# Kernel optimization log

Measured on AMD Instinct MI355X. Metric: run time of the kernel, lower is better.

Reference implementation:

```python
import jax, jax.numpy as jnp
import numpy as np

B, H, S, D = 4, 16, 2048, 64

def setup_inputs() -> dict:
    key = jax.random.key(0)
    kq, kk, kv = jax.random.split(key, 3)
    Q = jax.random.normal(kq, (B, H, S, D), dtype=jnp.float32)
    K = jax.random.normal(kk, (B, H, S, D), dtype=jnp.float32)
    V = jax.random.normal(kv, (B, H, S, D), dtype=jnp.float32)
    return {"Q": Q, "K": K, "V": V}

def reference(Q, K, V):
    d = Q.shape[-1]
    scale = jnp.sqrt(jnp.asarray(d, dtype=Q.dtype))
    # scores: [B, H, S, S]
    scores = jnp.einsum('bhqd,bhkd->bhqk', Q, K) / scale
    attn = jax.nn.softmax(scores, axis=-1)
    out = jnp.einsum('bhqk,bhkd->bhqd', attn, V)  # [B,H,S,D]
    # permute to [B,S,H,D] then merge heads -> [B,S,H*D]
    b, h, s, dd = out.shape
    return out.transpose(0, 2, 1, 3).reshape(b, s, h * dd)
```

## Files before the change

kernel.cpp:

```cpp
#include <hip/hip_runtime.h>
#include <hip/hip_bf16.h>


#define B_ 4
#define H_ 16
#define S_ 2048
#define D_ 64
#define BH 64
#define NKT 32
#define TILE_USH 4096
#define ARR_USH ((size_t)BH * NKT * TILE_USH)
#define WS_NEED (2 * ARR_USH * 2)
#define QSCALE 0.18033688011112042f

typedef float  f4 __attribute__((ext_vector_type(4)));
typedef short  s4 __attribute__((ext_vector_type(4)));
typedef short  s8 __attribute__((ext_vector_type(8)));
typedef unsigned short ushort_t;

__device__ __forceinline__ unsigned short f2bf(float x) {
  unsigned int u = __float_as_uint(x);
  u += 0x7fffu + ((u >> 16) & 1u);
  return (unsigned short)(u >> 16);
}
__device__ __forceinline__ unsigned int pk_bf16(float a, float b) {
  __hip_bfloat162 h = __float22bfloat162_rn(make_float2(a, b));
  union { __hip_bfloat162 h2; unsigned int u; } cv; cv.h2 = h; return cv.u;
}
__device__ __forceinline__ void splitbf_rne(float x, unsigned short& hi, unsigned short& lo) {
  hi = f2bf(x);
  float hf = __uint_as_float((unsigned int)hi << 16);
  lo = f2bf(x - hf);
}
__device__ __forceinline__ void splitbf(float x, unsigned short& hi, unsigned short& lo) {
  unsigned int u = __float_as_uint(x);
  hi = (unsigned short)(u >> 16);
  float hf = __uint_as_float(u & 0xffff0000u);
  lo = (unsigned short)(__float_as_uint(x - hf) >> 16);
}

typedef __attribute__((address_space(1))) const unsigned int* gas_t;
typedef __attribute__((address_space(3))) unsigned int* las_t;
__device__ __forceinline__ void gl_lds16(const void* g, void* l) {
  __builtin_amdgcn_global_load_lds((gas_t)g, (las_t)l, 16, 0, 0);
}

__global__ __launch_bounds__(256)
void prep(const float* __restrict__ K, const float* __restrict__ V,
          ushort_t* __restrict__ KH, ushort_t* __restrict__ VT) {
  __shared__ float Vf[64][68];
  const int tile = blockIdx.x;
  const int t = threadIdx.x;

  const float* vsrc = V + (size_t)tile * 4096;
  float4 vv[4];
  int srow[4], dcol[4];
  #pragma unroll
  for (int r = 0; r < 4; ++r) {
    int f = r * 256 + t; srow[r] = f >> 4; dcol[r] = (f & 15) << 2;
    vv[r] = *(const float4*)(vsrc + srow[r] * 64 + dcol[r]);
  }
  {
    const float* src0 = K + (size_t)tile * 4096;
    #pragma unroll
    for (int u = 0; u < 2; ++u) {
      unsigned int i = u * 256 + t;
      unsigned int row = i >> 3, c = (i & 7) ^ (row & 7);
      const float* src = src0 + row * 64 + c * 8;
      float4 a = *(const float4*)src;
      float4 b = *(const float4*)(src + 4);
      unsigned int d0 = pk_bf16(a.x, a.y), d1 = pk_bf16(a.z, a.w);
      unsigned int d2 = pk_bf16(b.x, b.y), d3 = pk_bf16(b.z, b.w);
      uint4 out = make_uint4(d0, d1, d2, d3);
      *(uint4*)(KH + (size_t)tile * TILE_USH + i * 8) = out;
    }
  }
  #pragma unroll
  for (int r = 0; r < 4; ++r) {
    int pcol = dcol[r] ^ (((srow[r] >> 3) & 3) << 2);
    *(float4*)&Vf[srow[r]][pcol] = vv[r];
  }
  __syncthreads();
  #pragma unroll
  for (int u = 0; u < 2; ++u) {
    unsigned int i = u * 256 + t;
    unsigned int drow = i >> 3, c = (i & 7) ^ (drow & 7);
    const unsigned int ka   = ((c >> 2) << 5) + ((c & 3) << 2);
    const unsigned int colA = drow ^ ((c & 2) << 1);
    const unsigned int colB = colA ^ 8;
    unsigned int d0 = pk_bf16(Vf[ka +  0][colA], Vf[ka +  1][colA]);
    unsigned int d1 = pk_bf16(Vf[ka +  2][colA], Vf[ka +  3][colA]);
    unsigned int d2 = pk_bf16(Vf[ka + 16][colB], Vf[ka + 17][colB]);
    unsigned int d3 = pk_bf16(Vf[ka + 18][colB], Vf[ka + 19][colB]);
    uint4 out = make_uint4(d0, d1, d2, d3);
    *(uint4*)(VT + (size_t)tile * TILE_USH + i * 8) = out;
  }
}

__global__ __launch_bounds__(256, 4)
void attn10(const float* __restrict__ Q, const ushort_t* __restrict__ KH,
            const ushort_t* __restrict__ VT, float* __restrict__ O) {
  __shared__ ushort_t KhS[2][TILE_USH];
  __shared__ ushort_t VtS[2][TILE_USH];

  const int t    = threadIdx.x;
  const int w    = t >> 6;
  const int lane = t & 63;
  const int g    = lane >> 4;
  const int ln   = lane & 15;

  const unsigned int n = blockIdx.x;
  const int bh = (int)((n >> 7) * 8 + (n & 7));
  const int q0 = (int)(((n >> 3) & 15) * 128);

  const size_t tb = (size_t)bh * NKT * TILE_USH;
  const unsigned int cb = w * 128;

  #pragma unroll
  for (int j = 0; j < 2; ++j) {
    const unsigned int ch = cb + 64u * j;
    const size_t go = tb + (size_t)(ch + lane) * 8;
    gl_lds16(KH + go, &KhS[0][ch * 8]);
    gl_lds16(VT + go, &VtS[0][ch * 8]);
  }

  s8 qfh[2][2], qfl[2][2];
  #pragma unroll
  for (int sub = 0; sub < 2; ++sub) {
    const int q = q0 + 32 * w + 16 * sub + ln;
    #pragma unroll
    for (int ks = 0; ks < 2; ++ks) {
      const float* qp = Q + ((size_t)bh * S_ + q) * 64 + 32 * ks + 8 * g;
      float4 a = *(const float4*)qp;
      float4 b = *(const float4*)(qp + 4);
      float xs[8] = {a.x, a.y, a.z, a.w, b.x, b.y, b.z, b.w};
      s8 hv, lv;
      #pragma unroll
      for (int j = 0; j < 8; ++j) {
        unsigned short h, lo; splitbf_rne(xs[j] * QSCALE, h, lo);
        hv[j] = (short)h; lv[j] = (short)lo;
      }
      qfh[sub][ks] = hv; qfl[sub][ks] = lv;
    }
  }

  f4 oacc[2][4];
  f4 lacc[2];
  #pragma unroll
  for (int s = 0; s < 2; ++s) {
    lacc[s] = (f4)0.0f;
    #pragma unroll
    for (int d = 0; d < 4; ++d) oacc[s][d] = (f4)0.0f;
  }

  s8 ones;
  #pragma unroll
  for (int j = 0; j < 8; ++j) ones[j] = (short)0x3F80;

  unsigned int foff[2];
  #pragma unroll
  for (int ks = 0; ks < 2; ++ks)
    foff[ks] = (unsigned)ln * 128u + (unsigned)(((4 * ks + g) ^ (ln & 7)) * 16);

  for (int kt = 0; kt < NKT; ++kt) {
    const int cur = kt & 1;
    __syncthreads();

    if (kt + 1 < NKT) {
      const size_t tbase = tb + (size_t)(kt + 1) * TILE_USH;
      const int nb = cur ^ 1;
      #pragma unroll
      for (int j = 0; j < 2; ++j) {
        const unsigned int ch = cb + 64u * j;
        const size_t go = tbase + (size_t)(ch + lane) * 8;
        gl_lds16(KH + go, &KhS[nb][ch * 8]);
        gl_lds16(VT + go, &VtS[nb][ch * 8]);
      }
    }

    const char* khb = (const char*)&KhS[cur][0];
    const char* vtb = (const char*)&VtS[cur][0];

    #pragma unroll
    for (int h = 0; h < 2; ++h) {
      s8 k00 = *(const s8*)(khb + (2 * h + 0) * 2048 + foff[0]);
      s8 k01 = *(const s8*)(khb + (2 * h + 0) * 2048 + foff[1]);
      s8 k10 = *(const s8*)(khb + (2 * h + 1) * 2048 + foff[0]);
      s8 k11 = *(const s8*)(khb + (2 * h + 1) * 2048 + foff[1]);

      s8 pa[2];
      #pragma unroll
      for (int sub = 0; sub < 2; ++sub) {
        f4 s0 = (f4)0.0f, s1 = (f4)0.0f;
        s0 = __builtin_amdgcn_mfma_f32_16x16x32_bf16(k00, qfh[sub][0], s0, 0, 0, 0);
        s0 = __builtin_amdgcn_mfma_f32_16x16x32_bf16(k00, qfl[sub][0], s0, 0, 0, 0);
        s0 = __builtin_amdgcn_mfma_f32_16x16x32_bf16(k01, qfh[sub][1], s0, 0, 0, 0);
        s0 = __builtin_amdgcn_mfma_f32_16x16x32_bf16(k01, qfl[sub][1], s0, 0, 0, 0);
        s1 = __builtin_amdgcn_mfma_f32_16x16x32_bf16(k10, qfh[sub][0], s1, 0, 0, 0);
        s1 = __builtin_amdgcn_mfma_f32_16x16x32_bf16(k10, qfl[sub][0], s1, 0, 0, 0);
        s1 = __builtin_amdgcn_mfma_f32_16x16x32_bf16(k11, qfh[sub][1], s1, 0, 0, 0);
        s1 = __builtin_amdgcn_mfma_f32_16x16x32_bf16(k11, qfl[sub][1], s1, 0, 0, 0);

        unsigned int a0 = pk_bf16(__builtin_amdgcn_exp2f(s0[0]),
                                  __builtin_amdgcn_exp2f(s0[1]));
        unsigned int a1 = pk_bf16(__builtin_amdgcn_exp2f(s0[2]),
                                  __builtin_amdgcn_exp2f(s0[3]));
        unsigned int b0 = pk_bf16(__builtin_amdgcn_exp2f(s1[0]),
                                  __builtin_amdgcn_exp2f(s1[1]));
        unsigned int b1 = pk_bf16(__builtin_amdgcn_exp2f(s1[2]),
                                  __builtin_amdgcn_exp2f(s1[3]));
        union { unsigned int u[4]; s8 v; } cvp;
        cvp.u[0] = a0; cvp.u[1] = a1; cvp.u[2] = b0; cvp.u[3] = b1;
        pa[sub] = cvp.v;
        lacc[sub] = __builtin_amdgcn_mfma_f32_16x16x32_bf16(pa[sub], ones, lacc[sub], 0, 0, 0);
      }

      #pragma unroll
      for (int dt = 0; dt < 4; ++dt) {
        s8 vb = *(const s8*)(vtb + dt * 2048 + foff[h]);
        #pragma unroll
        for (int sub = 0; sub < 2; ++sub)
          oacc[sub][dt] = __builtin_amdgcn_mfma_f32_16x16x32_bf16(pa[sub], vb, oacc[sub][dt], 0, 0, 0);
      }
    }
  }

  const int b = bh >> 4, hh = bh & 15;
  #pragma unroll
  for (int sub = 0; sub < 2; ++sub)
    #pragma unroll
    for (int r = 0; r < 4; ++r) {
      const float inv = 1.0f / lacc[sub][r];
      const int q = q0 + 32 * w + 16 * sub + 4 * g + r;
      float* dst = O + ((size_t)b * S_ + q) * (H_ * D_) + hh * 64;
      #pragma unroll
      for (int dt = 0; dt < 4; ++dt)
        dst[16 * dt + ln] = oacc[sub][dt][r] * inv;
    }
}

#define KQ_STR 72
#define VP_STR 76
__global__ __launch_bounds__(256, 2)
void attn_mfma(const float* __restrict__ Q, const float* __restrict__ K,
               const float* __restrict__ V, float* __restrict__ O) {
  __shared__ __align__(16) unsigned short Qh[64][KQ_STR];
  __shared__ __align__(16) unsigned short Ql[64][KQ_STR];
  __shared__ __align__(16) unsigned short Kh[64][KQ_STR];
  __shared__ __align__(16) unsigned short Kl[64][KQ_STR];
  __shared__ __align__(16) unsigned short Vt[64][VP_STR];
  __shared__ __align__(16) unsigned short Pb2[4][16][VP_STR];
  const int t = threadIdx.x, w = t >> 6, lane = t & 63, g = lane >> 4, ln = lane & 15;
  const int bh = blockIdx.x, q0 = blockIdx.y * 64;
  const size_t base = (size_t)bh * S_ * D_;
  {
    const float* Qg = Q + base + (size_t)q0 * D_;
    #pragma unroll
    for (int r = 0; r < 4; ++r) {
      int f = r * 256 + t, row = f >> 4, c4 = (f & 15) << 2;
      float4 v = *(const float4*)(Qg + row * 64 + c4);
      s4 hv, lv; unsigned short hb, lb;
      splitbf(v.x * 0.125f, hb, lb); hv[0] = (short)hb; lv[0] = (short)lb;
      splitbf(v.y * 0.125f, hb, lb); hv[1] = (short)hb; lv[1] = (short)lb;
      splitbf(v.z * 0.125f, hb, lb); hv[2] = (short)hb; lv[2] = (short)lb;
      splitbf(v.w * 0.125f, hb, lb); hv[3] = (short)hb; lv[3] = (short)lb;
      *(s4*)&Qh[row][c4] = hv; *(s4*)&Ql[row][c4] = lv;
    }
  }
  __syncthreads();
  s8 qfh[2], qfl[2];
  #pragma unroll
  for (int ks = 0; ks < 2; ++ks) {
    qfh[ks] = *(const s8*)&Qh[16 * w + ln][ks * 32 + 8 * g];
    qfl[ks] = *(const s8*)&Ql[16 * w + ln][ks * 32 + 8 * g];
  }
  f4 oacc[4]; float m[4], l[4];
  #pragma unroll
  for (int i = 0; i < 4; ++i) { oacc[i] = (f4)0.0f; m[i] = -1e30f; l[i] = 0.0f; }
  const float* Kg = K + base; const float* Vg = V + base;
  float4 kreg[4], vreg[4];
  #pragma unroll
  for (int r = 0; r < 4; ++r) {
    int f = r * 256 + t, row = f >> 4, c4 = (f & 15) << 2;
    kreg[r] = *(const float4*)(Kg + row * 64 + c4);
  }
  #pragma unroll
  for (int j = 0; j < 2; ++j) {
    int it = j * 256 + t, kp = it >> 4, c4 = (it & 15) << 2;
    vreg[2 * j] = *(const float4*)(Vg + (2 * kp) * 64 + c4);
    vreg[2 * j + 1] = *(const float4*)(Vg + (2 * kp + 1) * 64 + c4);
  }
  for (int kt = 0; kt < S_ / 64; ++kt) {
    __syncthreads();
    #pragma unroll
    for (int r = 0; r < 4; ++r) {
      int f = r * 256 + t, row = f >> 4, c4 = (f & 15) << 2;
      float4 v = kreg[r];
      s4 hv, lv; unsigned short hb, lb;
      splitbf(v.x, hb, lb); hv[0] = (short)hb; lv[0] = (short)lb;
      splitbf(v.y, hb, lb); hv[1] = (short)hb; lv[1] = (short)lb;
      splitbf(v.z, hb, lb); hv[2] = (short)hb; lv[2] = (short)lb;
      splitbf(v.w, hb, lb); hv[3] = (short)hb; lv[3] = (short)lb;
      *(s4*)&Kh[row][c4] = hv; *(s4*)&Kl[row][c4] = lv;
    }
    #pragma unroll
    for (int j = 0; j < 2; ++j) {
      int it = j * 256 + t, kp = it >> 4, c4 = (it & 15) << 2;
      float4 a = vreg[2 * j], b = vreg[2 * j + 1];
      float xa[4] = {a.x, a.y, a.z, a.w}, xb[4] = {b.x, b.y, b.z, b.w};
      #pragma unroll
      for (int i = 0; i < 4; ++i) {
        unsigned int pk = (unsigned int)f2bf(xa[i]) | ((unsigned int)f2bf(xb[i]) << 16);
        *(unsigned int*)&Vt[c4 + i][2 * kp] = pk;
      }
    }
    if (kt + 1 < S_ / 64) {
      const float* Kt = Kg + (size_t)(kt + 1) * 4096;
      const float* Vn = Vg + (size_t)(kt + 1) * 4096;
      #pragma unroll
      for (int r = 0; r < 4; ++r) {
        int f = r * 256 + t, row = f >> 4, c4 = (f & 15) << 2;
        kreg[r] = *(const float4*)(Kt + row * 64 + c4);
      }
      #pragma unroll
      for (int j = 0; j < 2; ++j) {
        int it = j * 256 + t, kp = it >> 4, c4 = (it & 15) << 2;
        vreg[2 * j] = *(const float4*)(Vn + (2 * kp) * 64 + c4);
        vreg[2 * j + 1] = *(const float4*)(Vn + (2 * kp + 1) * 64 + c4);
      }
    }
    __syncthreads();
    f4 sacc[4];
    #pragma unroll
    for (int nt = 0; nt < 4; ++nt) sacc[nt] = (f4)0.0f;
    #pragma unroll
    for (int nt = 0; nt < 4; ++nt)
      #pragma unroll
      for (int ks = 0; ks < 2; ++ks) {
        s8 kh = *(const s8*)&Kh[16 * nt + ln][ks * 32 + 8 * g];
        s8 kl = *(const s8*)&Kl[16 * nt + ln][ks * 32 + 8 * g];
        sacc[nt] = __builtin_amdgcn_mfma_f32_16x16x32_bf16(qfh[ks], kh, sacc[nt], 0, 0, 0);
        sacc[nt] = __builtin_amdgcn_mfma_f32_16x16x32_bf16(qfl[ks], kh, sacc[nt], 0, 0, 0);
        sacc[nt] = __builtin_amdgcn_mfma_f32_16x16x32_bf16(qfh[ks], kl, sacc[nt], 0, 0, 0);
      }
    #pragma unroll
    for (int r = 0; r < 4; ++r) {
      float rm = fmaxf(fmaxf(sacc[0][r], sacc[1][r]), fmaxf(sacc[2][r], sacc[3][r]));
      rm = fmaxf(rm, __shfl_xor(rm, 1)); rm = fmaxf(rm, __shfl_xor(rm, 2));
      rm = fmaxf(rm, __shfl_xor(rm, 4)); rm = fmaxf(rm, __shfl_xor(rm, 8));
      float mn = fmaxf(m[r], rm);
      float alpha = __expf(m[r] - mn); m[r] = mn;
      float p0 = __expf(sacc[0][r] - mn), p1 = __expf(sacc[1][r] - mn);
      float p2 = __expf(sacc[2][r] - mn), p3 = __expf(sacc[3][r] - mn);
      float rs = p0 + p1 + p2 + p3;
      rs += __shfl_xor(rs, 1); rs += __shfl_xor(rs, 2);
      rs += __shfl_xor(rs, 4); rs += __shfl_xor(rs, 8);
      l[r] = l[r] * alpha + rs;
      oacc[0][r] *= alpha; oacc[1][r] *= alpha; oacc[2][r] *= alpha; oacc[3][r] *= alpha;
      const int row = 4 * g + r;
      Pb2[w][row][ln] = f2bf(p0); Pb2[w][row][ln + 16] = f2bf(p1);
      Pb2[w][row][ln + 32] = f2bf(p2); Pb2[w][row][ln + 48] = f2bf(p3);
    }
    #pragma unroll
    for (int ks = 0; ks < 2; ++ks) {
      s4 pa0 = *(const s4*)&Pb2[w][ln][ks * 32 + 8 * g];
      s4 pa1 = *(const s4*)&Pb2[w][ln][ks * 32 + 8 * g + 4];
      s8 pa = __builtin_shufflevector(pa0, pa1, 0, 1, 2, 3, 4, 5, 6, 7);
      #pragma unroll
      for (int dt = 0; dt < 4; ++dt) {
        s4 vb0 = *(const s4*)&Vt[16 * dt + ln][ks * 32 + 8 * g];
        s4 vb1 = *(const s4*)&Vt[16 * dt + ln][ks * 32 + 8 * g + 4];
        s8 vb = __builtin_shufflevector(vb0, vb1, 0, 1, 2, 3, 4, 5, 6, 7);
        oacc[dt] = __builtin_amdgcn_mfma_f32_16x16x32_bf16(pa, vb, oacc[dt], 0, 0, 0);
      }
    }
  }
  const int b = bh >> 4, h = bh & 15;
  #pragma unroll
  for (int r = 0; r < 4; ++r) {
    const int q = q0 + 16 * w + 4 * g + r;
    const float inv = 1.0f / l[r];
    float* dst = O + ((size_t)b * S_ + q) * (H_ * D_) + h * 64;
    #pragma unroll
    for (int dt = 0; dt < 4; ++dt) dst[16 * dt + ln] = oacc[dt][r] * inv;
  }
}

extern "C" void kernel_launch(void* const* d_in, const int* in_sizes, int n_in,
                              void* d_out, int out_size, void* d_ws, size_t ws_size,
                              hipStream_t stream) {
  const float* Q = (const float*)d_in[0];
  const float* K = (const float*)d_in[1];
  const float* V = (const float*)d_in[2];
  float* Out = (float*)d_out;
  if (ws_size >= WS_NEED) {
    ushort_t* KHp = (ushort_t*)d_ws;
    ushort_t* VTp = KHp + ARR_USH;
    hipLaunchKernelGGL(prep, dim3(2048), dim3(256), 0, stream, K, V, KHp, VTp);
    hipLaunchKernelGGL(attn10, dim3(1024), dim3(256), 0, stream, Q, KHp, VTp, Out);
  } else {
    hipLaunchKernelGGL(attn_mfma, dim3(BH, S_ / 64), dim3(256), 0, stream, Q, K, V, Out);
  }
}
```

Before: 214.2 us.

## Software-pipeline QK and PV halves and raise wave priority around MFMA blocks

Restructures the per-tile inner loop so the QK^T MFMAs for the second key half are issued before the exp2/pack of the first half finishes feeding PV. This interleaves transcendental VALU work with independent MFMA chains. It also wraps each MFMA cluster in s_setprio(1)/s_setprio(0) so the arbiter favours matrix issue across co-resident waves. Holding SA and SB together raises register pressure, which could spill or lower occupancy under the 4-wave launch bound.

```diff
diff --git a/kernel.cpp b/kernel.cpp
--- a/kernel.cpp
+++ b/kernel.cpp
@@ -37,6 +37,10 @@
   hi = (unsigned short)(u >> 16);
   float hf = __uint_as_float(u & 0xffff0000u);
   lo = (unsigned short)(__float_as_uint(x - hf) >> 16);
+}
+
+__device__ __forceinline__ f4 mf(s8 a, s8 b, f4 c) {
+  return __builtin_amdgcn_mfma_f32_16x16x32_bf16(a, b, c, 0, 0, 0);
 }
 
 typedef __attribute__((address_space(1))) const unsigned int* gas_t;
@@ -98,7 +102,7 @@
 }
 
 __global__ __launch_bounds__(256, 4)
-void attn10(const float* __restrict__ Q, const ushort_t* __restrict__ KH,
+void attn11(const float* __restrict__ Q, const ushort_t* __restrict__ KH,
             const ushort_t* __restrict__ VT, float* __restrict__ O) {
   __shared__ ushort_t KhS[2][TILE_USH];
   __shared__ ushort_t VtS[2][TILE_USH];
@@ -181,47 +185,105 @@
     const char* khb = (const char*)&KhS[cur][0];
     const char* vtb = (const char*)&VtS[cur][0];
 
-    #pragma unroll
-    for (int h = 0; h < 2; ++h) {
-      s8 k00 = *(const s8*)(khb + (2 * h + 0) * 2048 + foff[0]);
-      s8 k01 = *(const s8*)(khb + (2 * h + 0) * 2048 + foff[1]);
-      s8 k10 = *(const s8*)(khb + (2 * h + 1) * 2048 + foff[0]);
-      s8 k11 = *(const s8*)(khb + (2 * h + 1) * 2048 + foff[1]);
-
-      s8 pa[2];
+    f4 SA[2][2], SB[2][2];
+    s8 paA[2], paB[2];
+
+    {
+      s8 k0 = *(const s8*)(khb + 0 * 2048 + foff[0]);
+      s8 k1 = *(const s8*)(khb + 0 * 2048 + foff[1]);
+      s8 k2 = *(const s8*)(khb + 1 * 2048 + foff[0]);
+      s8 k3 = *(const s8*)(khb + 1 * 2048 + foff[1]);
+      __builtin_amdgcn_s_setprio(1);
       #pragma unroll
       for (int sub = 0; sub < 2; ++sub) {
-        f4 s0 = (f4)0.0f, s1 = (f4)0.0f;
-        s0 = __builtin_amdgcn_mfma_f32_16x16x32_bf16(k00, qfh[sub][0], s0, 0, 0, 0);
-        s0 = __builtin_amdgcn_mfma_f32_16x16x32_bf16(k00, qfl[sub][0], s0, 0, 0, 0);
-        s0 = __builtin_amdgcn_mfma_f32_16x16x32_bf16(k01, qfh[sub][1], s0, 0, 0, 0);
-        s0 = __builtin_amdgcn_mfma_f32_16x16x32_bf16(k01, qfl[sub][1], s0, 0, 0, 0);
-        s1 = __builtin_amdgcn_mfma_f32_16x16x32_bf16(k10, qfh[sub][0], s1, 0, 0, 0);
-        s1 = __builtin_amdgcn_mfma_f32_16x16x32_bf16(k10, qfl[sub][0], s1, 0, 0, 0);
-        s1 = __builtin_amdgcn_mfma_f32_16x16x32_bf16(k11, qfh[sub][1], s1, 0, 0, 0);
-        s1 = __builtin_amdgcn_mfma_f32_16x16x32_bf16(k11, qfl[sub][1], s1, 0, 0, 0);
-
-        unsigned int a0 = pk_bf16(__builtin_amdgcn_exp2f(s0[0]),
-                                  __builtin_amdgcn_exp2f(s0[1]));
-        unsigned int a1 = pk_bf16(__builtin_amdgcn_exp2f(s0[2]),
-                                  __builtin_amdgcn_exp2f(s0[3]));
-        unsigned int b0 = pk_bf16(__builtin_amdgcn_exp2f(s1[0]),
-                                  __builtin_amdgcn_exp2f(s1[1]));
-        unsigned int b1 = pk_bf16(__builtin_amdgcn_exp2f(s1[2]),
-                                  __builtin_amdgcn_exp2f(s1[3]));
-        union { unsigned int u[4]; s8 v; } cvp;
-        cvp.u[0] = a0; cvp.u[1] = a1; cvp.u[2] = b0; cvp.u[3] = b1;
-        pa[sub] = cvp.v;
-        lacc[sub] = __builtin_amdgcn_mfma_f32_16x16x32_bf16(pa[sub], ones, lacc[sub], 0, 0, 0);
-      }
-
+        f4 x0 = (f4)0.0f, x1 = (f4)0.0f;
+        x0 = mf(k0, qfh[sub][0], x0); x0 = mf(k0, qfl[sub][0], x0);
+        x0 = mf(k1, qfh[sub][1], x0); x0 = mf(k1, qfl[sub][1], x0);
+        x1 = mf(k2, qfh[sub][0], x1); x1 = mf(k2, qfl[sub][0], x1);
+        x1 = mf(k3, qfh[sub][1], x1); x1 = mf(k3, qfl[sub][1], x1);
+        SA[sub][0] = x0; SA[sub][1] = x1;
+      }
+      __builtin_amdgcn_s_setprio(0);
+    }
+
+    #pragma unroll
+    for (int sub = 0; sub < 2; ++sub) {
+      f4 x0 = SA[sub][0], x1 = SA[sub][1];
+      unsigned int a0 = pk_bf16(__builtin_amdgcn_exp2f(x0[0]),
+                                __builtin_amdgcn_exp2f(x0[1]));
+      unsigned int a1 = pk_bf16(__builtin_amdgcn_exp2f(x0[2]),
+                                __builtin_amdgcn_exp2f(x0[3]));
+      unsigned int b0 = pk_bf16(__builtin_amdgcn_exp2f(x1[0]),
+                                __builtin_amdgcn_exp2f(x1[1]));
+      unsigned int b1 = pk_bf16(__builtin_amdgcn_exp2f(x1[2]),
+                                __builtin_amdgcn_exp2f(x1[3]));
+      union { unsigned int u[4]; s8 v; } cvp;
+      cvp.u[0] = a0; cvp.u[1] = a1; cvp.u[2] = b0; cvp.u[3] = b1;
+      paA[sub] = cvp.v;
+    }
+
+    {
+      s8 k0 = *(const s8*)(khb + 2 * 2048 + foff[0]);
+      s8 k1 = *(const s8*)(khb + 2 * 2048 + foff[1]);
+      s8 k2 = *(const s8*)(khb + 3 * 2048 + foff[0]);
+      s8 k3 = *(const s8*)(khb + 3 * 2048 + foff[1]);
+      __builtin_amdgcn_s_setprio(1);
+      #pragma unroll
+      for (int sub = 0; sub < 2; ++sub) {
+        f4 x0 = (f4)0.0f, x1 = (f4)0.0f;
+        x0 = mf(k0, qfh[sub][0], x0); x0 = mf(k0, qfl[sub][0], x0);
+        x0 = mf(k1, qfh[sub][1], x0); x0 = mf(k1, qfl[sub][1], x0);
+        x1 = mf(k2, qfh[sub][0], x1); x1 = mf(k2, qfl[sub][0], x1);
+        x1 = mf(k3, qfh[sub][1], x1); x1 = mf(k3, qfl[sub][1], x1);
+        SB[sub][0] = x0; SB[sub][1] = x1;
+      }
+      __builtin_amdgcn_s_setprio(0);
+    }
+
+    {
+      __builtin_amdgcn_s_setprio(1);
+      #pragma unroll
+      for (int sub = 0; sub < 2; ++sub)
+        lacc[sub] = mf(paA[sub], ones, lacc[sub]);
       #pragma unroll
       for (int dt = 0; dt < 4; ++dt) {
-        s8 vb = *(const s8*)(vtb + dt * 2048 + foff[h]);
+        s8 vb = *(const s8*)(vtb + dt * 2048 + foff[0]);
         #pragma unroll
         for (int sub = 0; sub < 2; ++sub)
-          oacc[sub][dt] = __builtin_amdgcn_mfma_f32_16x16x32_bf16(pa[sub], vb, oacc[sub][dt], 0, 0, 0);
-      }
+          oacc[sub][dt] = mf(paA[sub], vb, oacc[sub][dt]);
+      }
+      __builtin_amdgcn_s_setprio(0);
+    }
+
+    #pragma unroll
+    for (int sub = 0; sub < 2; ++sub) {
+      f4 x0 = SB[sub][0], x1 = SB[sub][1];
+      unsigned int a0 = pk_bf16(__builtin_amdgcn_exp2f(x0[0]),
+                                __builtin_amdgcn_exp2f(x0[1]));
+      unsigned int a1 = pk_bf16(__builtin_amdgcn_exp2f(x0[2]),
+                                __builtin_amdgcn_exp2f(x0[3]));
+      unsigned int b0 = pk_bf16(__builtin_amdgcn_exp2f(x1[0]),
+                                __builtin_amdgcn_exp2f(x1[1]));
+      unsigned int b1 = pk_bf16(__builtin_amdgcn_exp2f(x1[2]),
+                                __builtin_amdgcn_exp2f(x1[3]));
+      union { unsigned int u[4]; s8 v; } cvp;
+      cvp.u[0] = a0; cvp.u[1] = a1; cvp.u[2] = b0; cvp.u[3] = b1;
+      paB[sub] = cvp.v;
+    }
+
+    {
+      __builtin_amdgcn_s_setprio(1);
+      #pragma unroll
+      for (int sub = 0; sub < 2; ++sub)
+        lacc[sub] = mf(paB[sub], ones, lacc[sub]);
+      #pragma unroll
+      for (int dt = 0; dt < 4; ++dt) {
+        s8 vb = *(const s8*)(vtb + dt * 2048 + foff[1]);
+        #pragma unroll
+        for (int sub = 0; sub < 2; ++sub)
+          oacc[sub][dt] = mf(paB[sub], vb, oacc[sub][dt]);
+      }
+      __builtin_amdgcn_s_setprio(0);
     }
   }
 
@@ -397,7 +459,7 @@
     ushort_t* KHp = (ushort_t*)d_ws;
     ushort_t* VTp = KHp + ARR_USH;
     hipLaunchKernelGGL(prep, dim3(2048), dim3(256), 0, stream, K, V, KHp, VTp);
-    hipLaunchKernelGGL(attn10, dim3(1024), dim3(256), 0, stream, Q, KHp, VTp, Out);
+    hipLaunchKernelGGL(attn11, dim3(1024), dim3(256), 0, stream, Q, KHp, VTp, Out);
   } else {
     hipLaunchKernelGGL(attn_mfma, dim3(BH, S_ / 64), dim3(256), 0, stream, Q, K, V, Out);
   }
```

After: 216.2 us. About the same (+0.9%).
